# Kernel optimization log

Hardware: AMD Instinct MI355X
Metric: run time of the kernel (lower is better)

Reference implementation:

```python
import jax, jax.numpy as jnp
import numpy as np

T, C, NH, NL, NP = 5, 192, 4, 5, 4
DH = C // NH

def leaky(x):
    return jnp.where(x >= 0, x, 0.1 * x)

def conv2d(x, w, b, padding=1, dilation=1):
    out = jax.lax.conv_general_dilated(
        x, w, window_strides=(1, 1),
        padding=[(padding, padding), (padding, padding)],
        rhs_dilation=(dilation, dilation),
        dimension_numbers=('NCHW', 'OIHW', 'NCHW'))
    return out + b[None, :, None, None]

def grid_sample_border(img, gx, gy):
    # align_corners=True, padding_mode='border'; gx/gy normalized [-1,1], shape (B,H,W)
    B, Cc, H, W = img.shape
    x = jnp.clip((gx + 1.0) * 0.5 * (W - 1), 0.0, W - 1)
    y = jnp.clip((gy + 1.0) * 0.5 * (H - 1), 0.0, H - 1)
    x0 = jnp.floor(x); y0 = jnp.floor(y)
    wx = (x - x0).reshape(B, 1, -1); wy = (y - y0).reshape(B, 1, -1)
    flat = img.reshape(B, Cc, H * W)
    def g(yi, xi):
        xi = jnp.clip(xi, 0, W - 1).astype(jnp.int32)
        yi = jnp.clip(yi, 0, H - 1).astype(jnp.int32)
        return jnp.take_along_axis(flat, (yi * W + xi).reshape(B, 1, -1), axis=2)
    out = (g(y0, x0) * (1 - wx) * (1 - wy) + g(y0, x0 + 1) * wx * (1 - wy)
         + g(y0 + 1, x0) * (1 - wx) * wy + g(y0 + 1, x0 + 1) * wx * wy)
    return out.reshape(B, Cc, H, W)

def warp(x, flo):
    B, _, H, W = x.shape
    xx = jnp.arange(W, dtype=jnp.float32)[None, :] * jnp.ones((H, 1), jnp.float32)
    yy = jnp.arange(H, dtype=jnp.float32)[:, None] * jnp.ones((1, W), jnp.float32)
    gx = 2.0 * (xx[None] + flo[:, 0]) / max(W - 1, 1) - 1.0
    gy = 2.0 * (yy[None] + flo[:, 1]) / max(H - 1, 1) - 1.0
    return grid_sample_border(x, gx, gy)

def deform_sample(v_img, loc):
    # v_img (N,D,H,W); loc (N,Q,P,2) in [0,1]; bilinear, zeros padding, align_corners=False
    N, D, H, W = v_img.shape
    Q, P = loc.shape[1], loc.shape[2]
    x = loc[..., 0] * W - 0.5
    y = loc[..., 1] * H - 0.5
    x0 = jnp.floor(x); y0 = jnp.floor(y)
    wx = (x - x0).reshape(N, 1, -1); wy = (y - y0).reshape(N, 1, -1)
    flat = v_img.reshape(N, D, H * W)
    def g(yi, xi):
        valid = ((xi >= 0) & (xi <= W - 1) & (yi >= 0) & (yi <= H - 1)).astype(v_img.dtype)
        xi_c = jnp.clip(xi, 0, W - 1).astype(jnp.int32)
        yi_c = jnp.clip(yi, 0, H - 1).astype(jnp.int32)
        return jnp.take_along_axis(flat, (yi_c * W + xi_c).reshape(N, 1, -1), axis=2) * valid.reshape(N, 1, -1)
    out = (g(y0, x0) * (1 - wx) * (1 - wy) + g(y0, x0 + 1) * wx * (1 - wy)
         + g(y0 + 1, x0) * (1 - wx) * wy + g(y0 + 1, x0 + 1) * wx * wy)
    return out.reshape(N, D, Q, P)

def _forward(frame, srcframe, flow_forward, flow_backward,
             w_qk, b_qk, w_v, b_v, w_vproj, b_vproj, w_off, b_off,
             w_attn, b_attn, w_out, b_out, w_ff, b_ff,
             w_ffn1, b_ffn1, w_ffn2, b_ffn2):
    b, t, c, h, w = frame.shape
    ff01, ff12 = flow_forward[:, 0], flow_forward[:, 1]
    fb32, fb43 = flow_backward[:, 2], flow_backward[:, 3]
    ff02 = ff01 + warp(ff12, ff01)
    fb42 = fb43 + warp(fb32, fb43)
    warp02 = warp(frame[:, 0], ff02)
    warp12 = warp(frame[:, 1], ff12)
    warp32 = warp(frame[:, 3], fb32)
    warp42 = warp(frame[:, 4], fb42)
    qk_in = jnp.concatenate([warp02, warp12, frame[:, 2], warp32, warp42,
                             flow_forward.reshape(b, -1, h, w),
                             flow_backward.reshape(b, -1, h, w)], axis=1)
    queries = leaky(conv2d(qk_in, w_qk, b_qk)).reshape(b, t, c, h, w)
    value = leaky(conv2d(frame.reshape(b, t * c, h, w), w_v, b_v)).reshape(b, t, c, h, w)

    Lq = t * h * w
    q_tok = queries.transpose(0, 1, 3, 4, 2).reshape(b, Lq, c)
    v_tok = value.transpose(0, 1, 3, 4, 2).reshape(b, Lq, c)
    v_proj = (v_tok @ w_vproj.T + b_vproj).reshape(b, t, h * w, NH, DH)

    offs = (q_tok @ w_off.T + b_off).reshape(b, Lq, NH, NL, NP, 2)
    aw = (q_tok @ w_attn.T + b_attn).reshape(b, Lq, NH, NL * NP)
    aw = jax.nn.softmax(aw, axis=-1).reshape(b, Lq, NH, NL, NP)

    # reference points (all valid ratios are ones): ((x+0.5)/W, (y+0.5)/H)
    rx = (jnp.arange(w, dtype=frame.dtype) + 0.5) / w
    ry = (jnp.arange(h, dtype=frame.dtype) + 0.5) / h
    ref = jnp.stack(jnp.meshgrid(rx, ry, indexing='xy'), axis=-1).reshape(h * w, 2)
    ref = jnp.tile(ref, (t, 1))  # (Lq, 2)

    norm = jnp.array([w, h], dtype=frame.dtype)
    # flow-guided per-level displacement toward the center frame (level 2)
    zero = jnp.zeros_like(ff12)
    flows = jnp.stack([ff02, ff12, zero, fb32, fb42], axis=1)  # (b,NL,2,h,w)
    flow_norm = (flows / norm[None, None, :, None, None]).transpose(0, 1, 3, 4, 2).reshape(b, NL, h * w, 2)
    flow_norm = jnp.tile(flow_norm.transpose(0, 2, 1, 3), (1, t, 1, 1))  # (b,Lq,NL,2)

    loc = (ref[None, :, None, None, None, :]
           + offs / norm[None, None, None, None, None, :]
           + flow_norm[:, :, None, :, None, :])  # (b,Lq,NH,NL,NP,2)

    acc = jnp.zeros((b * NH, DH, Lq), dtype=frame.dtype)
    for l in range(NL):
        v_l = v_proj[:, l].transpose(0, 2, 3, 1).reshape(b * NH, DH, h, w)
        loc_l = loc[:, :, :, l].transpose(0, 2, 1, 3, 4).reshape(b * NH, Lq, NP, 2)
        samp = deform_sample(v_l, loc_l)  # (b*NH, DH, Lq, NP)
        w_l = aw[:, :, :, l].transpose(0, 2, 1, 3).reshape(b * NH, 1, Lq, NP)
        acc = acc + (samp * w_l).sum(-1)
    attn = acc.reshape(b, NH, DH, Lq).transpose(0, 3, 1, 2).reshape(b, Lq, c)
    attn = attn @ w_out.T + b_out

    out = attn.reshape(b, t, h, w, c).transpose(0, 1, 4, 2, 3).reshape(b * t, c, h, w)
    out = conv2d(out, w_ff, b_ff)
    out = out.reshape(b, t, c, h, w) + frame
    seq_in = jnp.concatenate([out.reshape(b * t, c, h, w), srcframe.reshape(b * t, c, h, w)], axis=1)
    ffn = conv2d(seq_in, w_ffn1, b_ffn1, padding=2, dilation=2)
    ffn = conv2d(leaky(ffn), w_ffn2, b_ffn2)
    out = out.reshape(b * t, c, h, w) + ffn
    return out.reshape(b, t, c, h, w)

def setup_inputs():
    key = jax.random.key(0)
    ks = jax.random.split(key, 16)
    B, H, W = 2, 64, 64
    s = 0.02
    d = {}
    d['frame'] = jax.random.normal(ks[0], (B, T, C, H, W), jnp.float32)
    d['srcframe'] = jax.random.normal(ks[1], (B, T, C, H, W), jnp.float32)
    d['flow_forward'] = jax.random.normal(ks[2], (B, 4, 2, H, W), jnp.float32)
    d['flow_backward'] = jax.random.normal(ks[3], (B, 4, 2, H, W), jnp.float32)
    cin_qk = T * C + 4 * (T - 1)
    d['w_qk'] = jax.random.normal(ks[4], (T * C, cin_qk, 3, 3), jnp.float32) * s
    d['b_qk'] = jnp.zeros((T * C,), jnp.float32)
    d['w_v'] = jax.random.normal(ks[5], (T * C, T * C, 3, 3), jnp.float32) * s
    d['b_v'] = jnp.zeros((T * C,), jnp.float32)
    d['w_vproj'] = jax.random.normal(ks[6], (C, C), jnp.float32) * s
    d['b_vproj'] = jnp.zeros((C,), jnp.float32)
    d['w_off'] = jax.random.normal(ks[7], (NH * NL * NP * 2, C), jnp.float32) * s
    d['b_off'] = jax.random.normal(ks[8], (NH * NL * NP * 2,), jnp.float32)
    d['w_attn'] = jax.random.normal(ks[9], (NH * NL * NP, C), jnp.float32) * s
    d['b_attn'] = jnp.zeros((NH * NL * NP,), jnp.float32)
    d['w_out'] = jax.random.normal(ks[10], (C, C), jnp.float32) * s
    d['b_out'] = jnp.zeros((C,), jnp.float32)
    d['w_ff'] = jax.random.normal(ks[11], (C, C, 3, 3), jnp.float32) * s
    d['b_ff'] = jnp.zeros((C,), jnp.float32)
    d['w_ffn1'] = jax.random.normal(ks[12], (C, 2 * C, 3, 3), jnp.float32) * s
    d['b_ffn1'] = jnp.zeros((C,), jnp.float32)
    d['w_ffn2'] = jax.random.normal(ks[13], (C, C, 3, 3), jnp.float32) * s
    d['b_ffn2'] = jnp.zeros((C,), jnp.float32)
    return d

def reference(frame, srcframe, flow_forward, flow_backward, w_qk, b_qk, w_v, b_v, w_vproj, b_vproj, w_off, b_off, w_attn, b_attn, w_out, b_out, w_ff, b_ff, w_ffn1, b_ffn1, w_ffn2, b_ffn2):
    out = _forward(frame, srcframe, flow_forward, flow_backward, w_qk, b_qk, w_v, b_v, w_vproj, b_vproj, w_off, b_off, w_attn, b_attn, w_out, b_out, w_ff, b_ff, w_ffn1, b_ffn1, w_ffn2, b_ffn2)
    return (out, srcframe)
```

## Files before the change

kernel.cpp:

```cpp
#include <hip/hip_runtime.h>


#define HWPX 4096
#define PPXN 4624
#define LQ   20480

typedef __attribute__((ext_vector_type(8))) short  short8;
typedef __attribute__((ext_vector_type(4))) short  short4v;
typedef __attribute__((ext_vector_type(4))) float  f32x4;

__device__ __forceinline__ unsigned short f2bf(float f) {
    unsigned u = __float_as_uint(f);
    unsigned r = (u + 0x7FFF + ((u >> 16) & 1)) >> 16;
    return (unsigned short)r;
}
__device__ __forceinline__ float bf2f(unsigned short s) {
    return __uint_as_float(((unsigned)s) << 16);
}

__device__ __forceinline__ void gl_lds16(const unsigned short* g, unsigned short* l) {
    __builtin_amdgcn_global_load_lds(
        (const __attribute__((address_space(1))) unsigned int*)g,
        (__attribute__((address_space(3))) unsigned int*)l, 16, 0, 0);
}

__device__ __forceinline__ float bsample(const float* __restrict__ p, float sx, float sy) {
    sx = fminf(fmaxf(sx, 0.f), 63.f);
    sy = fminf(fmaxf(sy, 0.f), 63.f);
    float x0 = floorf(sx), y0 = floorf(sy);
    int ix0 = (int)x0, iy0 = (int)y0;
    int ix1 = ix0 < 63 ? ix0 + 1 : 63;
    int iy1 = iy0 < 63 ? iy0 + 1 : 63;
    float wx = sx - x0, wy = sy - y0;
    float v00 = p[iy0*64+ix0], v01 = p[iy0*64+ix1];
    float v10 = p[iy1*64+ix0], v11 = p[iy1*64+ix1];
    return (v00*(1.f-wx) + v01*wx)*(1.f-wy) + (v10*(1.f-wx) + v11*wx)*wy;
}

__global__ __launch_bounds__(256) void k_flow(const float* __restrict__ ff,
                                              const float* __restrict__ fb,
                                              float* __restrict__ flows) {
    int i = blockIdx.x*256 + threadIdx.x;
    int b = i >> 12, pix = i & 4095;
    int x = pix & 63, y = pix >> 6;
    const float* ff01 = ff + (size_t)(b*4+0)*2*HWPX;
    const float* ff12 = ff + (size_t)(b*4+1)*2*HWPX;
    const float* fb32 = fb + (size_t)(b*4+2)*2*HWPX;
    const float* fb43 = fb + (size_t)(b*4+3)*2*HWPX;
    float* F = flows + (size_t)b*5*2*HWPX;
    float ax = ff01[pix], ay = ff01[HWPX+pix];
    float sx = bsample(ff12,      (float)x+ax, (float)y+ay);
    float sy = bsample(ff12+HWPX, (float)x+ax, (float)y+ay);
    F[0*2*HWPX + pix]        = ax + sx;
    F[0*2*HWPX + HWPX + pix] = ay + sy;
    F[1*2*HWPX + pix]        = ff12[pix];
    F[1*2*HWPX + HWPX + pix] = ff12[HWPX+pix];
    F[2*2*HWPX + pix]        = 0.f;
    F[2*2*HWPX + HWPX + pix] = 0.f;
    F[3*2*HWPX + pix]        = fb32[pix];
    F[3*2*HWPX + HWPX + pix] = fb32[HWPX+pix];
    float bx = fb43[pix], by = fb43[HWPX+pix];
    float tx = bsample(fb32,      (float)x+bx, (float)y+by);
    float ty = bsample(fb32+HWPX, (float)x+bx, (float)y+by);
    F[4*2*HWPX + pix]        = bx + tx;
    F[4*2*HWPX + HWPX + pix] = by + ty;
}

__global__ void k_qkin(const unsigned short* __restrict__ Pv,
                       const float* __restrict__ ff, const float* __restrict__ fb,
                       const float* __restrict__ flows,
                       unsigned short* __restrict__ Pqk)
{
    int ppx = blockIdx.x*64 + threadIdx.x;
    if (ppx >= PPXN) return;
    int b = blockIdx.z;
    int c8 = (blockIdx.y*4 + threadIdx.y)*8;
    unsigned short* dst = Pqk + ((size_t)b*PPXN + ppx)*992 + c8;
    int py = ppx/68, pxc = ppx - py*68;
    short8 o = {};
    if (py >= 2 && py < 66 && pxc >= 2 && pxc < 66 && c8 < 976) {
        int y = py-2, x = pxc-2, pix = (y<<6)+x;
        if (c8 >= 960) {
            #pragma unroll
            for (int j = 0; j < 8; ++j) {
                int k = c8 - 960 + j;
                float v = (k < 8) ? ff[((size_t)b*8 + k)*HWPX + pix]
                                  : fb[((size_t)b*8 + k - 8)*HWPX + pix];
                o[j] = (short)f2bf(v);
            }
        } else {
            const unsigned short* Pvb = Pv + (size_t)b*PPXN*960;
            int slot = c8/192;
            if (slot == 2) {
                o = *(const short8*)(Pvb + (size_t)ppx*960 + c8);
            } else {
                const float* F = flows + ((size_t)(b*5 + slot)*2)*HWPX;
                float sx = fminf(fmaxf((float)x + F[pix], 0.f), 63.f);
                float sy = fminf(fmaxf((float)y + F[HWPX + pix], 0.f), 63.f);
                float x0 = floorf(sx), y0 = floorf(sy);
                int ix0 = (int)x0, iy0 = (int)y0;
                int ix1 = ix0 < 63 ? ix0+1 : 63, iy1 = iy0 < 63 ? iy0+1 : 63;
                float wx = sx - x0, wy = sy - y0;
                float w00 = (1.f-wx)*(1.f-wy), w01 = wx*(1.f-wy);
                float w10 = (1.f-wx)*wy,       w11 = wx*wy;
                short8 v00 = *(const short8*)(Pvb + ((size_t)((iy0+2)*68 + ix0+2))*960 + c8);
                short8 v01 = *(const short8*)(Pvb + ((size_t)((iy0+2)*68 + ix1+2))*960 + c8);
                short8 v10 = *(const short8*)(Pvb + ((size_t)((iy1+2)*68 + ix0+2))*960 + c8);
                short8 v11 = *(const short8*)(Pvb + ((size_t)((iy1+2)*68 + ix1+2))*960 + c8);
                #pragma unroll
                for (int j = 0; j < 8; ++j) {
                    float v = bf2f((unsigned short)v00[j])*w00 + bf2f((unsigned short)v01[j])*w01
                            + bf2f((unsigned short)v10[j])*w10 + bf2f((unsigned short)v11[j])*w11;
                    o[j] = (short)f2bf(v);
                }
            }
        }
    }
    *(short8*)dst = o;
}

__global__ void t_pad(const float* __restrict__ in, unsigned short* __restrict__ outb,
                      int CI, int PITCH, int COFF)
{
    int ppx = blockIdx.x*64 + threadIdx.x;
    if (ppx >= PPXN) return;
    int img = blockIdx.z;
    int c8 = (blockIdx.y*4 + threadIdx.y)*8;
    unsigned short* dst = outb + ((size_t)img*PPXN + ppx)*PITCH;
    int py = ppx/68, pxc = ppx - py*68;
    if (py < 2 || py >= 66 || pxc < 2 || pxc >= 66) {
        short8 z = {};
        *(short8*)(dst + c8) = z;
        if (COFF) *(short8*)(dst + COFF + c8) = z;
        return;
    }
    int pix = ((py-2)<<6) + (pxc-2);
    short8 o;
    #pragma unroll
    for (int j = 0; j < 8; ++j)
        o[j] = (short)f2bf(in[((size_t)img*CI + c8 + j)*HWPX + pix]);
    *(short8*)(dst + COFF + c8) = o;
}

__global__ __launch_bounds__(256) void t_zb(unsigned short* __restrict__ buf, int PITCH) {
    int id = blockIdx.x*256 + threadIdx.x;
    int perpx = PITCH >> 3;
    int ppx = id / perpx, c8 = (id - ppx*perpx) * 8;
    if (ppx >= PPXN) return;
    int py = ppx/68, pxc = ppx - py*68;
    if (py >= 2 && py < 66 && pxc >= 2 && pxc < 66) return;
    short8 z = {};
    *(short8*)(buf + ((size_t)blockIdx.y*PPXN + ppx)*PITCH + c8) = z;
}

__global__ __launch_bounds__(256) void t_wT(const float* __restrict__ w,
                                            unsigned short* __restrict__ wT,
                                            int CI, int NKB) {
    int cotile = blockIdx.x, kblk = blockIdx.y;
    int tid = threadIdx.x & 255;
    unsigned short* dst = wT + ((size_t)(cotile*NKB + kblk))*18432;
    #pragma unroll
    for (int it = 0; it < 9; ++it) {
        int idx = it*256 + tid;
        int tap = idx >> 8, sub = idx & 255;
        int cg = sub >> 6, co = sub & 63;
        int cog = cotile*64 + co;
        int ci0 = kblk*32 + cg*8;
        short8 v;
        #pragma unroll
        for (int j = 0; j < 8; ++j) {
            int ci = ci0 + j;
            v[j] = (ci < CI) ? (short)f2bf(w[((size_t)cog*CI + ci)*9 + tap]) : (short)0;
        }
        *(short8*)(dst + (size_t)idx*8) = v;
    }
}

__global__ __launch_bounds__(256) void t_wg(const float* __restrict__ w1,
                                            const float* __restrict__ w2,
                                            unsigned short* __restrict__ wg,
                                            int co_split, int CO) {
    int cotile = blockIdx.x;
    int tid = threadIdx.x & 255;
    unsigned short* dst = wg + (size_t)cotile*12288;
    #pragma unroll
    for (int it = 0; it < 6; ++it) {
        int idx = it*256 + tid;
        int kblk = idx >> 8, sub = idx & 255;
        int cg = sub >> 6, co = sub & 63;
        int cog = cotile*64 + co;
        int ci0 = kblk*32 + cg*8;
        short8 v = {};
        if (cog < CO) {
            const float* row = (cog < co_split) ? w1 + (size_t)cog*192
                                                : w2 + (size_t)(cog - co_split)*192;
            #pragma unroll
            for (int j = 0; j < 8; ++j) v[j] = (short)f2bf(row[ci0 + j]);
        }
        *(short8*)(dst + (size_t)idx*8) = v;
    }
}

template<int ROWS, int DIL, int OMODE>
__global__ __launch_bounds__(256, 2) void k_conv(
    const unsigned short* __restrict__ P0, const unsigned short* __restrict__ P1,
    int CIP0, int CIP1, int NKB0, int NKB1,
    const unsigned short* __restrict__ wT0, const unsigned short* __restrict__ wT1,
    const float* __restrict__ bias0, const float* __restrict__ bias1,
    const float* __restrict__ res, float* __restrict__ outF,
    unsigned short* __restrict__ outB0, unsigned short* __restrict__ outB1,
    int njobs, int CO)
{
    constexpr int RR    = ROWS*4 + 2*DIL;
    constexpr int XP    = 64 + 2*DIL;
    constexpr int PLANE = RR*XP*16;
    constexpr int NCH   = RR*XP*4;
    constexpr int NXS   = (NCH + 255)/256;
    __shared__ unsigned char  s_x[4*PLANE];
    __shared__ unsigned short s_w[18432];

    int tid = threadIdx.x & 255;
    int gx = gridDim.x, gy = gridDim.y, gz = gridDim.z;
    int lin = blockIdx.x + gx*(blockIdx.y + gy*blockIdx.z);
    int tot = gx*gy*gz;
    if ((tot & 7) == 0) { int q = tot >> 3; lin = (lin & 7)*q + (lin >> 3); }
    int cotile = lin % gx; int rem = lin / gx;
    int ytile = rem % gy;  int z = rem / gy;

    int sel = (njobs == 2) ? (z >> 1) : 0;
    int img = (njobs == 2) ? (z & 1)  : z;
    const unsigned short* P  = sel ? P1  : P0;
    const unsigned short* wT = sel ? wT1 : wT0;
    const float* bias        = sel ? bias1 : bias0;
    unsigned short* outB     = sel ? outB1 : outB0;
    int CIP = sel ? CIP1 : CIP0;
    int NKB = sel ? NKB1 : NKB0;

    int y0 = ytile * (ROWS*4);
    const unsigned short* Pi = P + (size_t)img*PPXN*CIP;
    int w = tid >> 6, lane = tid & 63, lm = lane & 15, cig = lane >> 4;

    short8 xr[NXS];
    auto load_x = [&](int kb) {
        int k0 = kb*32;
        #pragma unroll
        for (int it = 0; it < NXS; ++it) {
            int li = it*256 + tid;
            if (li < NCH) {
                int p = li / (RR*XP), rm = li - p*(RR*XP);
                int r = rm / XP, c = rm - r*XP;
                xr[it] = *(const short8*)(Pi +
                    ((size_t)((y0 + 2 - DIL + r)*68 + c + 2 - DIL))*CIP + k0 + p*8);
            }
        }
    };
    auto write_x = [&]() {
        #pragma unroll
        for (int it = 0; it < NXS; ++it) {
            int li = it*256 + tid;
            if (li < NCH) {
                int p = li / (RR*XP), rm = li - p*(RR*XP);
                *(short8*)&s_x[p*PLANE + rm*16] = xr[it];
            }
        }
    };
    auto stage_w = [&](int kb) {
        const unsigned short* ws = wT + ((size_t)(cotile*NKB + kb))*18432;
        #pragma unroll
        for (int it = 0; it < 9; ++it)
            gl_lds16(ws + (size_t)(it*256+tid)*8, &s_w[(it*256+tid)*8]);
    };

    load_x(0); stage_w(0); write_x();
    __syncthreads();

    f32x4 acc[4][ROWS*4] = {};
    for (int kb = 0; kb < NKB; ++kb) {
        bool pf = (kb + 1 < NKB);
        if (pf) load_x(kb+1);
        #pragma unroll
        for (int t = 0; t < 9; ++t) {
            int ky = t/3, kx = t - ky*3;
            short8 A[4];
            #pragma unroll
            for (int mb = 0; mb < 4; ++mb)
                A[mb] = *(const short8*)&s_w[((t*4 + cig)*64 + mb*16 + lm)*8];
            #pragma unroll
            for (int s = 0; s < ROWS; ++s) {
                short8 Bf[4];
                #pragma unroll
                for (int nc = 0; nc < 4; ++nc)
                    Bf[nc] = *(const short8*)&s_x[cig*PLANE +
                               ((w*ROWS + s + ky*DIL)*XP + nc*16 + lm + kx*DIL)*16];
                #pragma unroll
                for (int mb = 0; mb < 4; ++mb)
                    #pragma unroll
                    for (int nc = 0; nc < 4; ++nc)
                        acc[mb][s*4+nc] = __builtin_amdgcn_mfma_f32_16x16x32_bf16(
                            A[mb], Bf[nc], acc[mb][s*4+nc], 0, 0, 0);
            }
        }
        __syncthreads();
        if (pf) { stage_w(kb+1); write_x(); }
        __syncthreads();
    }

    #pragma unroll
    for (int mb = 0; mb < 4; ++mb) {
        int cob = cotile*64 + mb*16 + cig*4;
        #pragma unroll
        for (int s = 0; s < ROWS; ++s) {
            int y = y0 + w*ROWS + s;
            #pragma unroll
            for (int nc = 0; nc < 4; ++nc) {
                int x = nc*16 + lm;
                int px = (y<<6) + x;
                float vv[4];
                #pragma unroll
                for (int r = 0; r < 4; ++r) {
                    float v = acc[mb][s*4+nc][r] + bias[cob + r];
                    if (OMODE == 0 || OMODE == 2) v = v >= 0.f ? v : 0.1f*v;
                    if (OMODE == 1 || OMODE == 3)
                        v += res[((size_t)img*192 + cob + r)*HWPX + px];
                    vv[r] = v;
                }
                if (OMODE == 0) {
                    int it = cob/192, cc = cob - it*192;
                    short4v sv;
                    #pragma unroll
                    for (int r = 0; r < 4; ++r) sv[r] = (short)f2bf(vv[r]);
                    *(short4v*)(outB + (((size_t)(img*5 + it)*HWPX + px)*192 + cc)) = sv;
                } else if (OMODE == 1) {
                    #pragma unroll
                    for (int r = 0; r < 4; ++r)
                        outF[((size_t)img*192 + cob + r)*HWPX + px] = vv[r];
                    int ppx = ((px>>6)+2)*68 + (px&63) + 2;
                    short4v sv;
                    #pragma unroll
                    for (int r = 0; r < 4; ++r) sv[r] = (short)f2bf(vv[r]);
                    *(short4v*)(outB + ((size_t)img*PPXN + ppx)*384 + cob) = sv;
                } else if (OMODE == 2) {
                    int ppx = ((px>>6)+2)*68 + (px&63) + 2;
                    short4v sv;
                    #pragma unroll
                    for (int r = 0; r < 4; ++r) sv[r] = (short)f2bf(vv[r]);
                    *(short4v*)(outB + ((size_t)img*PPXN + ppx)*192 + cob) = sv;
                } else {
                    #pragma unroll
                    for (int r = 0; r < 4; ++r)
                        outF[((size_t)img*192 + cob + r)*HWPX + px] = vv[r];
                }
            }
        }
    }
}

template<int GMODE>
__global__ __launch_bounds__(256) void k_gemmm(
    const unsigned short* __restrict__ X, const unsigned short* __restrict__ WG,
    const float* __restrict__ b1, const float* __restrict__ b2,
    float* __restrict__ o1, float* __restrict__ o2, unsigned short* __restrict__ ob)
{
    __shared__ unsigned char  s_x[2][4*4096];
    __shared__ unsigned short s_w[12288];
    int tid = threadIdx.x & 255;
    int cotile = blockIdx.x, pxt = blockIdx.y, img = blockIdx.z;
    int px0 = pxt*256;
    const unsigned short* Xi = X + (size_t)img*HWPX*192;
    #pragma unroll
    for (int it = 0; it < 6; ++it)
        gl_lds16(WG + (size_t)cotile*12288 + (it*256+tid)*8, &s_w[(it*256+tid)*8]);
    short8 xr[4];
    #pragma unroll
    for (int it = 0; it < 4; ++it)
        xr[it] = *(const short8*)(Xi + (size_t)(px0 + tid)*192 + it*8);
    #pragma unroll
    for (int it = 0; it < 4; ++it)
        *(short8*)&s_x[0][it*4096 + tid*16] = xr[it];
    __syncthreads();
    int w = tid >> 6, lane = tid & 63, lm = lane & 15, cig = lane >> 4;
    f32x4 acc[4][4] = {};
    int xb = 0;
    for (int kb = 0; kb < 6; ++kb) {
        bool pf = (kb < 5);
        if (pf) {
            int k0 = (kb+1)*32;
            #pragma unroll
            for (int it = 0; it < 4; ++it)
                xr[it] = *(const short8*)(Xi + (size_t)(px0 + tid)*192 + k0 + it*8);
        }
        short8 A[4], Bf[4];
        #pragma unroll
        for (int nb = 0; nb < 4; ++nb)
            Bf[nb] = *(const short8*)&s_x[xb][cig*4096 + (w*64 + nb*16 + lm)*16];
        #pragma unroll
        for (int mb = 0; mb < 4; ++mb)
            A[mb] = *(const short8*)&s_w[((kb*4 + cig)*64 + mb*16 + lm)*8];
        #pragma unroll
        for (int mb = 0; mb < 4; ++mb)
            #pragma unroll
            for (int nb = 0; nb < 4; ++nb)
                acc[mb][nb] = __builtin_amdgcn_mfma_f32_16x16x32_bf16(
                    A[mb], Bf[nb], acc[mb][nb], 0, 0, 0);
        if (pf) {
            #pragma unroll
            for (int it = 0; it < 4; ++it)
                *(short8*)&s_x[xb^1][it*4096 + tid*16] = xr[it];
        }
        __syncthreads();
        xb ^= 1;
    }
    int b = img/5, t = img - b*5;
    #pragma unroll
    for (int mb = 0; mb < 4; ++mb) {
        int cob = cotile*64 + mb*16 + cig*4;
        if (GMODE == 1 && cob >= 240) continue;
        #pragma unroll
        for (int nb = 0; nb < 4; ++nb) {
            int px = px0 + w*64 + nb*16 + lm;
            float vv[4];
            #pragma unroll
            for (int r = 0; r < 4; ++r) {
                float bv;
                if (GMODE == 1) bv = (cob + r < 160) ? b1[cob+r] : b2[cob+r-160];
                else bv = b1[cob + r];
                vv[r] = acc[mb][nb][r] + bv;
            }
            if (GMODE == 0) {
                int h = cob/48, d = cob - h*48;
                short4v s;
                #pragma unroll
                for (int r = 0; r < 4; ++r) s[r] = (short)f2bf(vv[r]);
                *(short4v*)(ob + (((size_t)img*4 + h)*HWPX + px)*48 + d) = s;
            } else if (GMODE == 1) {
                #pragma unroll
                for (int r = 0; r < 4; ++r) {
                    int co = cob + r;
                    if (co < 160) o1[((size_t)b*160 + co)*LQ + t*HWPX + px] = vv[r];
                    else          o2[((size_t)b*80 + co-160)*LQ + t*HWPX + px] = vv[r];
                }
            } else {
                int ppx = ((px>>6)+2)*68 + (px&63) + 2;
                short4v s;
                #pragma unroll
                for (int r = 0; r < 4; ++r) s[r] = (short)f2bf(vv[r]);
                *(short4v*)(ob + ((size_t)img*PPXN + ppx)*192 + cob) = s;
            }
        }
    }
}

__global__ __launch_bounds__(256) void k_softmax20(float* __restrict__ aw) {
    int i = blockIdx.x*256 + threadIdx.x;
    int lq = i % LQ;
    int bh = i / LQ;
    float* p = aw + (size_t)bh*20*LQ + lq;
    float e[20];
    float m = -1e30f;
    #pragma unroll
    for (int j = 0; j < 20; ++j) { e[j] = p[(size_t)j*LQ]; m = fmaxf(m, e[j]); }
    float s = 0.f;
    #pragma unroll
    for (int j = 0; j < 20; ++j) { e[j] = expf(e[j]-m); s += e[j]; }
    float inv = 1.f/s;
    #pragma unroll
    for (int j = 0; j < 20; ++j) p[(size_t)j*LQ] = e[j]*inv;
}

__device__ __forceinline__ void addtap(float* acc, const unsigned short* __restrict__ src, float w) {
    const short8* s8 = (const short8*)src;
    #pragma unroll
    for (int q = 0; q < 6; ++q) {
        short8 v = s8[q];
        #pragma unroll
        for (int j = 0; j < 8; ++j)
            acc[q*8+j] += w * bf2f((unsigned short)v[j]);
    }
}

__global__ __launch_bounds__(256) void k_sample(
    const unsigned short* __restrict__ vp, const float* __restrict__ offs,
    const float* __restrict__ aw, const float* __restrict__ flows,
    unsigned short* __restrict__ accout)
{
    int blk = blockIdx.x;
    int b = blk / 320, sub = blk - b*320;
    int h = threadIdx.x >> 6;
    int lq = sub*64 + (threadIdx.x & 63);
    int pix = lq & 4095;
    int x = pix & 63, y = pix >> 6;
    const float* offp = offs + ((size_t)b*160 + h*40)*LQ + lq;
    const float* awp  = aw   + ((size_t)b*80  + h*20)*LQ + lq;
    float acc[48];
    #pragma unroll
    for (int d = 0; d < 48; ++d) acc[d] = 0.f;

    for (int l = 0; l < 5; ++l) {
        float fx = flows[((size_t)(b*5+l)*2+0)*HWPX + pix];
        float fy = flows[((size_t)(b*5+l)*2+1)*HWPX + pix];
        const unsigned short* vpl = vp + ((size_t)(b*5+l)*4 + h)*HWPX*48;
        #pragma unroll
        for (int p = 0; p < 4; ++p) {
            int o = l*4 + p;
            float ox = offp[(size_t)(2*o)*LQ];
            float oy = offp[(size_t)(2*o+1)*LQ];
            float wv = awp[(size_t)o*LQ];
            float sx = (float)x + ox + fx;
            float sy = (float)y + oy + fy;
            float x0f = floorf(sx), y0f = floorf(sy);
            float wx = sx - x0f, wy = sy - y0f;
            int ix0 = (int)x0f, iy0 = (int)y0f;
            float w00 = wv*(1.f-wx)*(1.f-wy), w01 = wv*wx*(1.f-wy);
            float w10 = wv*(1.f-wx)*wy,       w11 = wv*wx*wy;
            bool vx0 = (ix0 >= 0)  && (ix0 <= 63);
            bool vx1 = (ix0 >= -1) && (ix0 <= 62);
            bool vy0 = (iy0 >= 0)  && (iy0 <= 63);
            bool vy1 = (iy0 >= -1) && (iy0 <= 62);
            if (vy0 && vx0) addtap(acc, vpl + (size_t)(iy0*64 + ix0)*48,       w00);
            if (vy0 && vx1) addtap(acc, vpl + (size_t)(iy0*64 + ix0 + 1)*48,   w01);
            if (vy1 && vx0) addtap(acc, vpl + (size_t)((iy0+1)*64 + ix0)*48,   w10);
            if (vy1 && vx1) addtap(acc, vpl + (size_t)((iy0+1)*64 + ix0+1)*48, w11);
        }
    }
    unsigned short* dst = accout + ((size_t)b*LQ + lq)*192 + h*48;
    #pragma unroll
    for (int q = 0; q < 6; ++q) {
        short8 s;
        #pragma unroll
        for (int j = 0; j < 8; ++j) s[j] = (short)f2bf(acc[q*8+j]);
        *(short8*)(dst + q*8) = s;
    }
}


extern "C" void kernel_launch(void* const* d_in, const int* in_sizes, int n_in,
                              void* d_out, int out_size, void* d_ws, size_t ws_size,
                              hipStream_t stream) {
    (void)in_sizes; (void)n_in; (void)out_size; (void)ws_size;
    const float* frame    = (const float*)d_in[0];
    const float* srcframe = (const float*)d_in[1];
    const float* flow_f   = (const float*)d_in[2];
    const float* flow_b   = (const float*)d_in[3];
    const float* w_qk  = (const float*)d_in[4];  const float* b_qk  = (const float*)d_in[5];
    const float* w_v   = (const float*)d_in[6];  const float* b_v   = (const float*)d_in[7];
    const float* w_vp  = (const float*)d_in[8];  const float* b_vp  = (const float*)d_in[9];
    const float* w_off = (const float*)d_in[10]; const float* b_off = (const float*)d_in[11];
    const float* w_at  = (const float*)d_in[12]; const float* b_at  = (const float*)d_in[13];
    const float* w_out = (const float*)d_in[14]; const float* b_out = (const float*)d_in[15];
    const float* w_ff  = (const float*)d_in[16]; const float* b_ff  = (const float*)d_in[17];
    const float* w_f1  = (const float*)d_in[18]; const float* b_f1  = (const float*)d_in[19];
    const float* w_f2  = (const float*)d_in[20]; const float* b_f2  = (const float*)d_in[21];
    float* out = (float*)d_out;
    char* W = (char*)d_ws;

    float*          flows  = (float*)(W + 0);
    unsigned short* wT_qk  = (unsigned short*)(W + 327680);
    unsigned short* wT_v   = (unsigned short*)(W + 17469440);
    unsigned short* wT_ff  = (unsigned short*)(W + 327680);
    unsigned short* wT_f1  = (unsigned short*)(W + 991232);
    unsigned short* wT_f2  = (unsigned short*)(W + 2318336);
    unsigned short* wg_vp  = (unsigned short*)(W + 2981888);
    unsigned short* wg_oa  = (unsigned short*)(W + 3055616);
    unsigned short* wg_out = (unsigned short*)(W + 3153920);
    unsigned short* P_qk   = (unsigned short*)(W + 34058240);
    unsigned short* P_ff   = P_qk;
    unsigned short* P_v    = (unsigned short*)(W + 52406272);
    unsigned short* P_mid  = P_v;
    unsigned short* Q_tok  = (unsigned short*)(W + 70162432);
    unsigned short* acc_tok= Q_tok;
    unsigned short* V_tok  = (unsigned short*)(W + 85891072);
    unsigned short* P_ffn1 = V_tok;
    unsigned short* vp     = (unsigned short*)(W + 101619712);
    float*          offs   = (float*)(W + 121403392);
    float*          aw     = (float*)(W + 147617792);
    float*          out1   = (float*)(W + 160724992);

    dim3 bp(64, 4);

    k_flow<<<32, 256, 0, stream>>>(flow_f, flow_b, flows);
    t_wT<<<dim3(15,31), 256, 0, stream>>>(w_qk, wT_qk, 976, 31);
    t_wT<<<dim3(15,30), 256, 0, stream>>>(w_v,  wT_v,  960, 30);
    t_pad<<<dim3(73,30,2), bp, 0, stream>>>(frame, P_v, 960, 960, 0);
    k_qkin<<<dim3(73,31,2), bp, 0, stream>>>(P_v, flow_f, flow_b, flows, P_qk);
    k_conv<2,1,0><<<dim3(15,8,4), 256, 0, stream>>>(
        P_qk, P_v, 992, 960, 31, 30, wT_qk, wT_v, b_qk, b_v,
        nullptr, nullptr, Q_tok, V_tok, 2, 960);
    t_wT<<<dim3(3,6),  256, 0, stream>>>(w_ff, wT_ff, 192, 6);
    t_wT<<<dim3(3,12), 256, 0, stream>>>(w_f1, wT_f1, 384, 12);
    t_wT<<<dim3(3,6),  256, 0, stream>>>(w_f2, wT_f2, 192, 6);
    t_wg<<<3, 256, 0, stream>>>(w_vp,  nullptr, wg_vp, 192, 192);
    t_wg<<<4, 256, 0, stream>>>(w_off, w_at,    wg_oa, 160, 240);
    t_wg<<<3, 256, 0, stream>>>(w_out, nullptr, wg_out, 192, 192);
    t_zb<<<dim3(434,10), 256, 0, stream>>>(P_ff, 192);
    t_zb<<<dim3(434,10), 256, 0, stream>>>(P_mid, 192);
    k_gemmm<0><<<dim3(3,16,10), 256, 0, stream>>>(V_tok, wg_vp, b_vp, nullptr,
                                                  nullptr, nullptr, vp);
    k_gemmm<1><<<dim3(4,16,10), 256, 0, stream>>>(Q_tok, wg_oa, b_off, b_at,
                                                  offs, aw, nullptr);
    k_softmax20<<<640, 256, 0, stream>>>(aw);
    k_sample<<<640, 256, 0, stream>>>(vp, offs, aw, flows, acc_tok);
    t_pad<<<dim3(73,6,10), bp, 0, stream>>>(srcframe, P_ffn1, 192, 384, 192);
    k_gemmm<2><<<dim3(3,16,10), 256, 0, stream>>>(acc_tok, wg_out, b_out, nullptr,
                                                  nullptr, nullptr, P_ff);
    k_conv<1,1,1><<<dim3(3,16,10), 256, 0, stream>>>(
        P_ff, nullptr, 192, 0, 6, 0, wT_ff, nullptr, b_ff, nullptr,
        frame, out1, P_ffn1, nullptr, 1, 192);
    k_conv<1,2,2><<<dim3(3,16,10), 256, 0, stream>>>(
        P_ffn1, nullptr, 384, 0, 12, 0, wT_f1, nullptr, b_f1, nullptr,
        nullptr, nullptr, P_mid, nullptr, 1, 192);
    k_conv<1,1,3><<<dim3(3,16,10), 256, 0, stream>>>(
        P_mid, nullptr, 192, 0, 6, 0, wT_f2, nullptr, b_f2, nullptr,
        out1, out, nullptr, nullptr, 1, 192);
    hipMemcpyAsync(out + (size_t)2*5*192*HWPX, srcframe,
                   (size_t)2*5*192*HWPX*sizeof(float),
                   hipMemcpyDeviceToDevice, stream);
}
```

Measured before the change: 871.3 us.

## Fuse softmax into sampler, register-stage conv weights, drop fp32 intermediate, retile FF convs

```diff
diff --git a/kernel.cpp b/kernel.cpp
--- a/kernel.cpp
+++ b/kernel.cpp
@@ -16,12 +16,6 @@
 }
 __device__ __forceinline__ float bf2f(unsigned short s) {
     return __uint_as_float(((unsigned)s) << 16);
-}
-
-__device__ __forceinline__ void gl_lds16(const unsigned short* g, unsigned short* l) {
-    __builtin_amdgcn_global_load_lds(
-        (const __attribute__((address_space(1))) unsigned int*)g,
-        (__attribute__((address_space(3))) unsigned int*)l, 16, 0, 0);
 }
 
 __device__ __forceinline__ float bsample(const float* __restrict__ p, float sx, float sy) {
@@ -142,15 +136,18 @@
     *(short8*)(dst + COFF + c8) = o;
 }
 
-__global__ __launch_bounds__(256) void t_zb(unsigned short* __restrict__ buf, int PITCH) {
+__global__ __launch_bounds__(256) void t_zb(unsigned short* __restrict__ b0,
+                                            unsigned short* __restrict__ b1) {
     int id = blockIdx.x*256 + threadIdx.x;
-    int perpx = PITCH >> 3;
-    int ppx = id / perpx, c8 = (id - ppx*perpx) * 8;
+    int ppx = id / 24, c8 = (id - ppx*24) * 8;
     if (ppx >= PPXN) return;
     int py = ppx/68, pxc = ppx - py*68;
     if (py >= 2 && py < 66 && pxc >= 2 && pxc < 66) return;
+    int y = blockIdx.y;
+    unsigned short* buf = (y < 10) ? b0 : b1;
+    int img = (y < 10) ? y : y - 10;
     short8 z = {};
-    *(short8*)(buf + ((size_t)blockIdx.y*PPXN + ppx)*PITCH + c8) = z;
+    *(short8*)(buf + ((size_t)img*PPXN + ppx)*192 + c8) = z;
 }
 
 __global__ __launch_bounds__(256) void t_wT(const float* __restrict__ w,
@@ -201,15 +198,16 @@
     }
 }
 
-template<int ROWS, int DIL, int OMODE>
+template<int ROWS, int DIL, int OUTK, bool LEAKY, int RESK>
 __global__ __launch_bounds__(256, 2) void k_conv(
     const unsigned short* __restrict__ P0, const unsigned short* __restrict__ P1,
     int CIP0, int CIP1, int NKB0, int NKB1,
     const unsigned short* __restrict__ wT0, const unsigned short* __restrict__ wT1,
     const float* __restrict__ bias0, const float* __restrict__ bias1,
-    const float* __restrict__ res, float* __restrict__ outF,
+    const float* __restrict__ resF, const unsigned short* __restrict__ resB, int resPitch,
+    float* __restrict__ outF,
     unsigned short* __restrict__ outB0, unsigned short* __restrict__ outB1,
-    int njobs, int CO)
+    int outPitch, int outCoff, int njobs)
 {
     constexpr int RR    = ROWS*4 + 2*DIL;
     constexpr int XP    = 64 + 2*DIL;
@@ -241,6 +239,7 @@
     int w = tid >> 6, lane = tid & 63, lm = lane & 15, cig = lane >> 4;
 
     short8 xr[NXS];
+    short8 wr[9];
     auto load_x = [&](int kb) {
         int k0 = kb*32;
         #pragma unroll
@@ -254,7 +253,13 @@
             }
         }
     };
-    auto write_x = [&]() {
+    auto load_w = [&](int kb) {
+        const unsigned short* ws = wT + ((size_t)(cotile*NKB + kb))*18432;
+        #pragma unroll
+        for (int it = 0; it < 9; ++it)
+            wr[it] = *(const short8*)(ws + (size_t)(it*256+tid)*8);
+    };
+    auto write_xw = [&]() {
         #pragma unroll
         for (int it = 0; it < NXS; ++it) {
             int li = it*256 + tid;
@@ -263,21 +268,19 @@
                 *(short8*)&s_x[p*PLANE + rm*16] = xr[it];
             }
         }
+        #pragma unroll
+        for (int it = 0; it < 9; ++it)
+            *(short8*)&s_w[(it*256+tid)*8] = wr[it];
     };
-    auto stage_w = [&](int kb) {
-        const unsigned short* ws = wT + ((size_t)(cotile*NKB + kb))*18432;
-        #pragma unroll
-        for (int it = 0; it < 9; ++it)
-            gl_lds16(ws + (size_t)(it*256+tid)*8, &s_w[(it*256+tid)*8]);
-    };
-
-    load_x(0); stage_w(0); write_x();
+
+    load_x(0); load_w(0); write_xw();
     __syncthreads();
 
     f32x4 acc[4][ROWS*4] = {};
     for (int kb = 0; kb < NKB; ++kb) {
         bool pf = (kb + 1 < NKB);
-        if (pf) load_x(kb+1);
+        if (pf) { load_x(kb+1); load_w(kb+1); }
+        __builtin_amdgcn_s_setprio(1);
         #pragma unroll
         for (int t = 0; t < 9; ++t) {
             int ky = t/3, kx = t - ky*3;
@@ -300,8 +303,9 @@
                             A[mb], Bf[nc], acc[mb][s*4+nc], 0, 0, 0);
             }
         }
+        __builtin_amdgcn_s_setprio(0);
         __syncthreads();
-        if (pf) { stage_w(kb+1); write_x(); }
+        if (pf) write_xw();
         __syncthreads();
     }
 
@@ -315,36 +319,30 @@
             for (int nc = 0; nc < 4; ++nc) {
                 int x = nc*16 + lm;
                 int px = (y<<6) + x;
+                int ppx = (y+2)*68 + x + 2;
                 float vv[4];
+                short4v rv;
+                if (RESK == 2)
+                    rv = *(const short4v*)(resB + ((size_t)img*PPXN + ppx)*resPitch + cob);
                 #pragma unroll
                 for (int r = 0; r < 4; ++r) {
                     float v = acc[mb][s*4+nc][r] + bias[cob + r];
-                    if (OMODE == 0 || OMODE == 2) v = v >= 0.f ? v : 0.1f*v;
-                    if (OMODE == 1 || OMODE == 3)
-                        v += res[((size_t)img*192 + cob + r)*HWPX + px];
+                    if (LEAKY) v = v >= 0.f ? v : 0.1f*v;
+                    if (RESK == 1) v += resF[((size_t)img*192 + cob + r)*HWPX + px];
+                    if (RESK == 2) v += bf2f((unsigned short)rv[r]);
                     vv[r] = v;
                 }
-                if (OMODE == 0) {
+                if (OUTK == 0) {
                     int it = cob/192, cc = cob - it*192;
                     short4v sv;
                     #pragma unroll
                     for (int r = 0; r < 4; ++r) sv[r] = (short)f2bf(vv[r]);
                     *(short4v*)(outB + (((size_t)(img*5 + it)*HWPX + px)*192 + cc)) = sv;
-                } else if (OMODE == 1) {
-                    #pragma unroll
-                    for (int r = 0; r < 4; ++r)
-                        outF[((size_t)img*192 + cob + r)*HWPX + px] = vv[r];
-                    int ppx = ((px>>6)+2)*68 + (px&63) + 2;
+                } else if (OUTK == 1) {
                     short4v sv;
                     #pragma unroll
                     for (int r = 0; r < 4; ++r) sv[r] = (short)f2bf(vv[r]);
-                    *(short4v*)(outB + ((size_t)img*PPXN + ppx)*384 + cob) = sv;
-                } else if (OMODE == 2) {
-                    int ppx = ((px>>6)+2)*68 + (px&63) + 2;
-                    short4v sv;
-                    #pragma unroll
-                    for (int r = 0; r < 4; ++r) sv[r] = (short)f2bf(vv[r]);
-                    *(short4v*)(outB + ((size_t)img*PPXN + ppx)*192 + cob) = sv;
+                    *(short4v*)(outB0 + ((size_t)img*PPXN + ppx)*outPitch + outCoff + cob) = sv;
                 } else {
                     #pragma unroll
                     for (int r = 0; r < 4; ++r)
@@ -367,13 +365,17 @@
     int cotile = blockIdx.x, pxt = blockIdx.y, img = blockIdx.z;
     int px0 = pxt*256;
     const unsigned short* Xi = X + (size_t)img*HWPX*192;
+    short8 wr[6];
     #pragma unroll
     for (int it = 0; it < 6; ++it)
-        gl_lds16(WG + (size_t)cotile*12288 + (it*256+tid)*8, &s_w[(it*256+tid)*8]);
+        wr[it] = *(const short8*)(WG + (size_t)cotile*12288 + (it*256+tid)*8);
     short8 xr[4];
     #pragma unroll
     for (int it = 0; it < 4; ++it)
         xr[it] = *(const short8*)(Xi + (size_t)(px0 + tid)*192 + it*8);
+    #pragma unroll
+    for (int it = 0; it < 6; ++it)
+        *(short8*)&s_w[(it*256+tid)*8] = wr[it];
     #pragma unroll
     for (int it = 0; it < 4; ++it)
         *(short8*)&s_x[0][it*4096 + tid*16] = xr[it];
@@ -450,23 +452,6 @@
     }
 }
 
-__global__ __launch_bounds__(256) void k_softmax20(float* __restrict__ aw) {
-    int i = blockIdx.x*256 + threadIdx.x;
-    int lq = i % LQ;
-    int bh = i / LQ;
-    float* p = aw + (size_t)bh*20*LQ + lq;
-    float e[20];
-    float m = -1e30f;
-    #pragma unroll
-    for (int j = 0; j < 20; ++j) { e[j] = p[(size_t)j*LQ]; m = fmaxf(m, e[j]); }
-    float s = 0.f;
-    #pragma unroll
-    for (int j = 0; j < 20; ++j) { e[j] = expf(e[j]-m); s += e[j]; }
-    float inv = 1.f/s;
-    #pragma unroll
-    for (int j = 0; j < 20; ++j) p[(size_t)j*LQ] = e[j]*inv;
-}
-
 __device__ __forceinline__ void addtap(float* acc, const unsigned short* __restrict__ src, float w) {
     const short8* s8 = (const short8*)src;
     #pragma unroll
@@ -491,6 +476,15 @@
     int x = pix & 63, y = pix >> 6;
     const float* offp = offs + ((size_t)b*160 + h*40)*LQ + lq;
     const float* awp  = aw   + ((size_t)b*80  + h*20)*LQ + lq;
+    float e[20];
+    float m = -1e30f;
+    #pragma unroll
+    for (int j = 0; j < 20; ++j) { e[j] = awp[(size_t)j*LQ]; m = fmaxf(m, e[j]); }
+    float ssum = 0.f;
+    #pragma unroll
+    for (int j = 0; j < 20; ++j) { e[j] = __expf(e[j]-m); ssum += e[j]; }
+    float inv = 1.f/ssum;
+
     float acc[48];
     #pragma unroll
     for (int d = 0; d < 48; ++d) acc[d] = 0.f;
@@ -504,7 +498,7 @@
             int o = l*4 + p;
             float ox = offp[(size_t)(2*o)*LQ];
             float oy = offp[(size_t)(2*o+1)*LQ];
-            float wv = awp[(size_t)o*LQ];
+            float wv = e[o]*inv;
             float sx = (float)x + ox + fx;
             float sy = (float)y + oy + fy;
             float x0f = floorf(sx), y0f = floorf(sy);
@@ -573,7 +567,6 @@
     unsigned short* vp     = (unsigned short*)(W + 101619712);
     float*          offs   = (float*)(W + 121403392);
     float*          aw     = (float*)(W + 147617792);
-    float*          out1   = (float*)(W + 160724992);
 
     dim3 bp(64, 4);
 
@@ -582,35 +575,33 @@
     t_wT<<<dim3(15,30), 256, 0, stream>>>(w_v,  wT_v,  960, 30);
     t_pad<<<dim3(73,30,2), bp, 0, stream>>>(frame, P_v, 960, 960, 0);
     k_qkin<<<dim3(73,31,2), bp, 0, stream>>>(P_v, flow_f, flow_b, flows, P_qk);
-    k_conv<2,1,0><<<dim3(15,8,4), 256, 0, stream>>>(
+    k_conv<2,1,0,true,0><<<dim3(15,8,4), 256, 0, stream>>>(
         P_qk, P_v, 992, 960, 31, 30, wT_qk, wT_v, b_qk, b_v,
-        nullptr, nullptr, Q_tok, V_tok, 2, 960);
+        nullptr, nullptr, 0, nullptr, Q_tok, V_tok, 0, 0, 2);
     t_wT<<<dim3(3,6),  256, 0, stream>>>(w_ff, wT_ff, 192, 6);
     t_wT<<<dim3(3,12), 256, 0, stream>>>(w_f1, wT_f1, 384, 12);
     t_wT<<<dim3(3,6),  256, 0, stream>>>(w_f2, wT_f2, 192, 6);
     t_wg<<<3, 256, 0, stream>>>(w_vp,  nullptr, wg_vp, 192, 192);
     t_wg<<<4, 256, 0, stream>>>(w_off, w_at,    wg_oa, 160, 240);
     t_wg<<<3, 256, 0, stream>>>(w_out, nullptr, wg_out, 192, 192);
-    t_zb<<<dim3(434,10), 256, 0, stream>>>(P_ff, 192);
-    t_zb<<<dim3(434,10), 256, 0, stream>>>(P_mid, 192);
+    t_zb<<<dim3(434,20), 256, 0, stream>>>(P_ff, P_mid);
     k_gemmm<0><<<dim3(3,16,10), 256, 0, stream>>>(V_tok, wg_vp, b_vp, nullptr,
                                                   nullptr, nullptr, vp);
     k_gemmm<1><<<dim3(4,16,10), 256, 0, stream>>>(Q_tok, wg_oa, b_off, b_at,
                                                   offs, aw, nullptr);
-    k_softmax20<<<640, 256, 0, stream>>>(aw);
     k_sample<<<640, 256, 0, stream>>>(vp, offs, aw, flows, acc_tok);
     t_pad<<<dim3(73,6,10), bp, 0, stream>>>(srcframe, P_ffn1, 192, 384, 192);
     k_gemmm<2><<<dim3(3,16,10), 256, 0, stream>>>(acc_tok, wg_out, b_out, nullptr,
                                                   nullptr, nullptr, P_ff);
-    k_conv<1,1,1><<<dim3(3,16,10), 256, 0, stream>>>(
+    k_conv<2,1,1,false,1><<<dim3(3,8,10), 256, 0, stream>>>(
         P_ff, nullptr, 192, 0, 6, 0, wT_ff, nullptr, b_ff, nullptr,
-        frame, out1, P_ffn1, nullptr, 1, 192);
-    k_conv<1,2,2><<<dim3(3,16,10), 256, 0, stream>>>(
+        frame, nullptr, 0, nullptr, P_ffn1, nullptr, 384, 0, 1);
+    k_conv<1,2,1,true,0><<<dim3(3,16,10), 256, 0, stream>>>(
         P_ffn1, nullptr, 384, 0, 12, 0, wT_f1, nullptr, b_f1, nullptr,
-        nullptr, nullptr, P_mid, nullptr, 1, 192);
-    k_conv<1,1,3><<<dim3(3,16,10), 256, 0, stream>>>(
+        nullptr, nullptr, 0, nullptr, P_mid, nullptr, 192, 0, 1);
+    k_conv<2,1,2,false,2><<<dim3(3,8,10), 256, 0, stream>>>(
         P_mid, nullptr, 192, 0, 6, 0, wT_f2, nullptr, b_f2, nullptr,
-        out1, out, nullptr, nullptr, 1, 192);
+        nullptr, P_ffn1, 384, out, nullptr, nullptr, 0, 0, 1);
     hipMemcpyAsync(out + (size_t)2*5*192*HWPX, srcframe,
                    (size_t)2*5*192*HWPX*sizeof(float),
                    hipMemcpyDeviceToDevice, stream);
```

New measurement: 1.185 ms. 36.0% more time.
